# Kernel tuning notes

Measured on AMD Instinct MI355X. Metric: run time of the kernel, lower is better.

The kernel has to match this reference:

```python
import jax, jax.numpy as jnp
import numpy as np

B, N, IN_DIM, MEM, HID = 8, 512, 768, 300, 64
LEAKY_SLOPE = 0.01
NEG_INF = -1e30


def setup_inputs() -> dict:
    key = jax.random.key(0)
    ks = jax.random.split(key, 8)
    adj = jax.random.randint(ks[0], (B, N, N), 0, 2).astype(jnp.float32)
    feature = jax.random.normal(ks[1], (B, N, IN_DIM), dtype=jnp.float32)
    # GCN projection W[0]: Linear(in_dim, mem_dim)
    W_w = jax.random.normal(ks[2], (MEM, IN_DIM), dtype=jnp.float32) / np.sqrt(IN_DIM)
    W_b = jax.random.normal(ks[3], (MEM,), dtype=jnp.float32) * 0.02
    # afcs: Linear(2*mem, hidden) -> ReLU -> Linear(hidden, 1)
    a1_w = jax.random.normal(ks[4], (HID, 2 * MEM), dtype=jnp.float32) / np.sqrt(2 * MEM)
    a1_b = jax.random.normal(ks[5], (HID,), dtype=jnp.float32) * 0.02
    a2_w = jax.random.normal(ks[6], (1, HID), dtype=jnp.float32) / np.sqrt(HID)
    a2_b = jax.random.normal(ks[7], (1,), dtype=jnp.float32) * 0.02
    return {"adj": adj, "feature": feature, "W_w": W_w, "W_b": W_b,
            "a1_w": a1_w, "a1_b": a1_b, "a2_w": a2_w, "a2_b": a2_b}


def reference(adj, feature, W_w, W_b, a1_w, a1_b, a2_w, a2_b):
    # num_layers = 1 -> single GAT layer, no inter-layer dropout (eval math)
    b, n, _ = adj.shape
    h = feature @ W_w.T + W_b                      # [B,N,MEM]
    # a_input[:, i*N+j] = concat(h_i, h_j); decompose Linear(2*mem, hid)
    s_i = h @ a1_w[:, :MEM].T                      # [B,N,HID] (contribution of h_i)
    s_j = h @ a1_w[:, MEM:].T                      # [B,N,HID] (contribution of h_j)
    pre = s_i[:, :, None, :] + s_j[:, None, :, :] + a1_b   # [B,N,N,HID]
    e = jax.nn.relu(pre) @ a2_w[0] + a2_b[0]       # [B,N,N] (second afcs linear)
    e = jnp.where(e >= 0, e, LEAKY_SLOPE * e)      # LeakyReLU(0.01)
    # mask_logits + softmax over the FLATTENED N*N dim (dim=1 of [B, N*N])
    dmask = adj.reshape(b, -1)
    logits = e.reshape(b, -1) * dmask + (1.0 - dmask) * NEG_INF
    attention = jax.nn.softmax(logits, axis=1).reshape(b, n, n)
    out = jnp.einsum('bij,bjd->bid', attention, h)  # attention.bmm(h)
    return out
```

## Files before the change

### kernel.cpp

```cpp
#include <hip/hip_runtime.h>

#define NEGINF (-1e30f)

typedef __attribute__((ext_vector_type(8))) short short8;
typedef __attribute__((ext_vector_type(4))) float f32x4;

__device__ inline float waveRedSum(float v){
  #pragma unroll
  for (int o = 32; o > 0; o >>= 1) v += __shfl_down(v, o, 64);
  return v;
}
__device__ inline float waveRedMax(float v){
  #pragma unroll
  for (int o = 32; o > 0; o >>= 1) v = fmaxf(v, __shfl_down(v, o, 64));
  return v;
}
__device__ inline float4 f4z(){ return make_float4(0.f,0.f,0.f,0.f); }
#define F4C(v, c) ((c)==0?(v).x:(c)==1?(v).y:(c)==2?(v).z:(v).w)

__device__ inline unsigned short f2bf(float f){
  unsigned u = __float_as_uint(f);
  unsigned r = u + 0x7fffu + ((u >> 16) & 1u);
  return (unsigned short)(r >> 16);
}
__device__ inline float bf2f(unsigned short h){
  return __uint_as_float(((unsigned)h) << 16);
}

__global__ __launch_bounds__(256) void k1_h(const float* __restrict__ A,
                                            const float* __restrict__ W,
                                            const float* __restrict__ Wb,
                                            float* __restrict__ H){
  __shared__ short Ah[2][64*40];
  __shared__ short Al[2][64*40];
  __shared__ short Bh[2][64*40];
  __shared__ short Bl[2][64*40];
  const int fid = blockIdx.x;
  const int wl  = (fid & 7) * 40 + (fid >> 3);
  const int y = wl / 5, x = wl % 5;
  const int m0 = y * 64, c0 = x * 64;
  const int t = threadIdx.x;
  const int lane = t & 63, w = t >> 6;
  const int wr = w >> 1, wc = w & 1;
  const int srow = t >> 2, kq = (t & 3) * 8;
  const bool bok = (c0 + srow) < 300;
  const float* Arow = A + (size_t)(m0 + srow) * 768 + kq;
  const float* Wrow = W + (size_t)(c0 + srow) * 768 + kq;
  float4 ra0, ra1, rb0, rb1;
#define K1_LD(kt) { \
    ra0 = *(const float4*)(Arow + (kt)); \
    ra1 = *(const float4*)(Arow + (kt) + 4); \
    rb0 = bok ? *(const float4*)(Wrow + (kt)) : f4z(); \
    rb1 = bok ? *(const float4*)(Wrow + (kt) + 4) : f4z(); }
  K1_LD(0)
  f32x4 acc[2][2];
  #pragma unroll
  for (int i = 0; i < 2; i++)
    #pragma unroll
    for (int j = 0; j < 2; j++)
      acc[i][j] = (f32x4){0.f, 0.f, 0.f, 0.f};
  const int fr = lane & 15;
  const int fk = (lane >> 4) * 8;
  int p = 0;
  for (int tile = 0; tile < 24; ++tile){
    {
      float av[8] = {ra0.x, ra0.y, ra0.z, ra0.w, ra1.x, ra1.y, ra1.z, ra1.w};
      float bv[8] = {rb0.x, rb0.y, rb0.z, rb0.w, rb1.x, rb1.y, rb1.z, rb1.w};
      short8 vah, val_, vbh, vbl;
      #pragma unroll
      for (int i = 0; i < 8; i++){
        unsigned short hh = f2bf(av[i]);
        vah[i] = (short)hh;
        val_[i] = (short)f2bf(av[i] - bf2f(hh));
        unsigned short gh = f2bf(bv[i]);
        vbh[i] = (short)gh;
        vbl[i] = (short)f2bf(bv[i] - bf2f(gh));
      }
      const int o = srow * 40 + kq;
      *(short8*)&Ah[p][o] = vah;
      *(short8*)&Al[p][o] = val_;
      *(short8*)&Bh[p][o] = vbh;
      *(short8*)&Bl[p][o] = vbl;
    }
    __syncthreads();
    if (tile < 23) K1_LD((tile + 1) * 32)
    {
      const int a0o = (wr*32      + fr) * 40 + fk;
      const int a1o = (wr*32 + 16 + fr) * 40 + fk;
      const int b0o = (wc*32      + fr) * 40 + fk;
      const int b1o = (wc*32 + 16 + fr) * 40 + fk;
      short8 fAh[2], fAl[2], fBh[2], fBl[2];
      fAh[0] = *(short8*)&Ah[p][a0o]; fAh[1] = *(short8*)&Ah[p][a1o];
      fAl[0] = *(short8*)&Al[p][a0o]; fAl[1] = *(short8*)&Al[p][a1o];
      fBh[0] = *(short8*)&Bh[p][b0o]; fBh[1] = *(short8*)&Bh[p][b1o];
      fBl[0] = *(short8*)&Bl[p][b0o]; fBl[1] = *(short8*)&Bl[p][b1o];
      #pragma unroll
      for (int sm = 0; sm < 2; sm++)
        #pragma unroll
        for (int sn = 0; sn < 2; sn++){
          acc[sm][sn] = __builtin_amdgcn_mfma_f32_16x16x32_bf16(fAh[sm], fBh[sn], acc[sm][sn], 0, 0, 0);
          acc[sm][sn] = __builtin_amdgcn_mfma_f32_16x16x32_bf16(fAh[sm], fBl[sn], acc[sm][sn], 0, 0, 0);
          acc[sm][sn] = __builtin_amdgcn_mfma_f32_16x16x32_bf16(fAl[sm], fBh[sn], acc[sm][sn], 0, 0, 0);
        }
    }
    p ^= 1;
  }
#undef K1_LD
  const int crow = (lane >> 4) * 4;
  const int ccol = lane & 15;
  #pragma unroll
  for (int sn = 0; sn < 2; sn++){
    const int gcol = c0 + wc*32 + sn*16 + ccol;
    if (gcol < 300){
      const float bi = Wb[gcol];
      #pragma unroll
      for (int sm = 0; sm < 2; sm++){
        const int rbase = m0 + wr*32 + sm*16 + crow;
        #pragma unroll
        for (int r = 0; r < 4; r++)
          H[(size_t)(rbase + r) * 300 + gcol] = acc[sm][sn][r] + bi;
      }
    }
  }
}

__global__ __launch_bounds__(256) void k2_s(const float* __restrict__ Hm,
                                            const float* __restrict__ a1w,
                                            const float* __restrict__ a1b,
                                            float* __restrict__ S){
  __shared__ float As[2][32*40];
  __shared__ float Bs[2][32*136];
  const int bid = blockIdx.x;
  const int y = (bid & 7) * 16 + (bid >> 3);
  const int m0 = y * 32;
  const int t = threadIdx.x;
  const int tr4 = (t >> 5) * 4, tc = t & 31;
  const int arow = t >> 3, akq = t & 7;
  const int bn = t & 127, bkh = t >> 7;
  const float* brp = (bn < 64) ? &a1w[(size_t)bn * 600] : &a1w[(size_t)(bn - 64) * 600 + 300];
  float4 ha, b4[4];
  float4 acc[4];
  #pragma unroll
  for (int i = 0; i < 4; i++) acc[i] = f4z();
#define K2_LD(kt) { \
    const int ka = (kt) + akq*4; \
    ha = (ka < 300) ? *(const float4*)&Hm[(size_t)(m0 + arow)*300 + ka] : f4z(); \
    _Pragma("unroll") \
    for (int j = 0; j < 4; j++){ \
      const int kb = (kt) + bkh*16 + 4*j; \
      b4[j] = (kb < 300) ? *(const float4*)&brp[kb] : f4z(); \
    } }
  K2_LD(0)
  int p = 0;
  for (int tile = 0; tile < 10; ++tile){
    #pragma unroll
    for (int jj = 0; jj < 4; jj++)
      As[p][(akq*4 + jj)*40 + ((((arow>>2) ^ akq) & 7) << 2) + (arow & 3)] = F4C(ha, jj);
    #pragma unroll
    for (int jj = 0; jj < 16; jj++){
      const int kl = bkh*16 + jj;
      const int swb = (kl >> 2) & 7;
      Bs[p][kl*136 + (((bn>>2) ^ swb) << 2) + (bn & 3)] = F4C(b4[jj>>2], jj&3);
    }
    __syncthreads();
    if (tile < 9) K2_LD((tile + 1) * 32)
    #pragma unroll
    for (int kk = 0; kk < 32; kk++){
      const int sw = (kk >> 2) & 7;
      const float4 av = *(const float4*)&As[p][kk*40 + (((t>>5) ^ sw) << 2)];
      const float4 bv = *(const float4*)&Bs[p][kk*136 + ((tc ^ sw) << 2)];
      acc[0].x += av.x*bv.x; acc[0].y += av.x*bv.y; acc[0].z += av.x*bv.z; acc[0].w += av.x*bv.w;
      acc[1].x += av.y*bv.x; acc[1].y += av.y*bv.y; acc[1].z += av.y*bv.z; acc[1].w += av.y*bv.w;
      acc[2].x += av.z*bv.x; acc[2].y += av.z*bv.y; acc[2].z += av.z*bv.z; acc[2].w += av.z*bv.w;
      acc[3].x += av.w*bv.x; acc[3].y += av.w*bv.y; acc[3].z += av.w*bv.z; acc[3].w += av.w*bv.w;
    }
    p ^= 1;
  }
#undef K2_LD
  const int tc4 = tc * 4;
  float4 bi = f4z();
  if (tc4 < 64) bi = *(const float4*)&a1b[tc4];
  #pragma unroll
  for (int i = 0; i < 4; i++){
    float4 o = make_float4(acc[i].x+bi.x, acc[i].y+bi.y, acc[i].z+bi.z, acc[i].w+bi.w);
    *(float4*)&S[(size_t)(m0 + tr4 + i) * 128 + tc4] = o;
  }
}

__global__ __launch_bounds__(256) void k3_logits(const float* __restrict__ S,
                                                 const float* __restrict__ adj,
                                                 const float* __restrict__ a2w,
                                                 const float* __restrict__ a2b,
                                                 float* __restrict__ L,
                                                 float* __restrict__ bm,
                                                 float* __restrict__ bs){
  __shared__ float sj_s[64*68];
  __shared__ float w_s[64];
  __shared__ float redm[4];
  __shared__ float reds[4];
  __shared__ float smax;
  const int b  = blockIdx.z;
  const int i0 = blockIdx.y * 32;
  const int j0 = blockIdx.x * 64;
  const int t  = threadIdx.x;
  const int j = t & 63, iq = t >> 6;
  if (t < 16) *(float4*)&w_s[t*4] = *(const float4*)&a2w[t*4];
  #pragma unroll
  for (int q = 0; q < 4; q++){
    int c = t + q*256; int r = c >> 4, c4 = c & 15;
    *(float4*)&sj_s[r*68 + c4*4] = *(const float4*)&S[(size_t)(b*512 + j0 + r)*128 + 64 + c4*4];
  }
  float vsi[8];
  #pragma unroll
  for (int r = 0; r < 8; r++)
    vsi[r] = S[(size_t)(b*512 + i0 + r*4 + iq) * 128 + j];
  __syncthreads();
  const float a2bv = a2b[0];
  float accA[8][4];
  #pragma unroll
  for (int r = 0; r < 8; r++)
    #pragma unroll
    for (int c = 0; c < 4; c++) accA[r][c] = 0.f;
  #pragma unroll
  for (int k4 = 0; k4 < 16; k4++){
    const float4 sj4 = *(const float4*)&sj_s[j*68 + k4*4];
    const float4 w4  = *(const float4*)&w_s[k4*4];
    #pragma unroll
    for (int c = 0; c < 4; c++){
      const int k = k4*4 + c;
      const float sjc = F4C(sj4, c);
      const float wc  = F4C(w4, c);
      #pragma unroll
      for (int r = 0; r < 8; r++){
        const float s = __int_as_float(__builtin_amdgcn_readlane(__float_as_int(vsi[r]), k));
        accA[r][c] += fmaxf(s + sjc, 0.f) * wc;
      }
    }
  }
  float l_arr[8];
  float locmax = -3e38f;
  #pragma unroll
  for (int r = 0; r < 8; r++){
    const int i = r*4 + iq;
    float e = ((accA[r][0] + accA[r][1]) + (accA[r][2] + accA[r][3])) + a2bv;
    e = (e >= 0.f) ? e : 0.01f * e;
    size_t idxg = (size_t)(b*512 + i0 + i)*512 + j0 + j;
    float l = (adj[idxg] != 0.f) ? e : NEGINF;
    l_arr[r] = l;
    L[idxg] = l;
    locmax = fmaxf(locmax, l);
  }
  float m = waveRedMax(locmax);
  if ((t & 63) == 0) redm[t >> 6] = m;
  __syncthreads();
  if (t == 0) smax = fmaxf(fmaxf(redm[0], redm[1]), fmaxf(redm[2], redm[3]));
  __syncthreads();
  const float mb = smax;
  float sacc = 0.f;
  #pragma unroll
  for (int r = 0; r < 8; r++) sacc += __expf(l_arr[r] - mb);
  sacc = waveRedSum(sacc);
  if ((t & 63) == 0) reds[t >> 6] = sacc;
  __syncthreads();
  if (t == 0){
    const int bid = (blockIdx.z * 16 + blockIdx.y) * 8 + blockIdx.x;
    bm[bid] = mb;
    bs[bid] = (reds[0] + reds[1]) + (reds[2] + reds[3]);
  }
}

__global__ __launch_bounds__(128) void k6_red(const float* __restrict__ bm,
                                              const float* __restrict__ bs,
                                              float* __restrict__ sums,
                                              float* __restrict__ maxg){
  const int b = blockIdx.x, t = threadIdx.x;
  const float m = bm[b*128 + t];
  float mm = waveRedMax(m);
  __shared__ float r2m[2];
  __shared__ float mgs;
  if ((t & 63) == 0) r2m[t >> 6] = mm;
  __syncthreads();
  if (t == 0) mgs = fmaxf(r2m[0], r2m[1]);
  __syncthreads();
  const float mg = mgs;
  float v = bs[b*128 + t] * __expf(m - mg);
  v = waveRedSum(v);
  __shared__ float r2s[2];
  if ((t & 63) == 0) r2s[t >> 6] = v;
  __syncthreads();
  if (t == 0){ sums[b] = r2s[0] + r2s[1]; maxg[b] = mg; }
}

__global__ __launch_bounds__(256) void k7_out(const float* __restrict__ Lr,
                                              const float* __restrict__ Hm,
                                              const float* __restrict__ sums,
                                              const float* __restrict__ maxg,
                                              float* __restrict__ out){
  __shared__ short Ah[2][64*40];
  __shared__ short Al[2][64*40];
  __shared__ short Bh[2][64*40];
  __shared__ short Bl[2][64*40];
  const int fid = blockIdx.x;
  const int b = fid & 7, idx = fid >> 3;
  const int y = idx / 5, x = idx % 5;
  const int m0 = y * 64, c0 = x * 64;
  const int t = threadIdx.x;
  const int lane = t & 63, wv = t >> 6;
  const int wr = wv >> 1, wc = wv & 1;
  const float mx = maxg[b];
  const int srow = t >> 2, kq = (t & 3) * 8;
  const float* Lrow = Lr + (size_t)(b*512 + m0 + srow) * 512 + kq;
  const int tk = t >> 4, tn = t & 15;
  const int k0 = tk * 2, n0 = tn * 4;
  const int gcolB = c0 + n0;
  const bool bok = gcolB < 300;
  float4 ra0, ra1, hb0, hb1;
#define K7_LD(kt) { \
    ra0 = *(const float4*)(Lrow + (kt)); \
    ra1 = *(const float4*)(Lrow + (kt) + 4); \
    const float* hr = Hm + (size_t)(b*512 + (kt) + k0) * 300 + gcolB; \
    hb0 = bok ? *(const float4*)hr : f4z(); \
    hb1 = bok ? *(const float4*)(hr + 300) : f4z(); }
  K7_LD(0)
  f32x4 acc[2][2];
  #pragma unroll
  for (int i = 0; i < 2; i++)
    #pragma unroll
    for (int jj = 0; jj < 2; jj++)
      acc[i][jj] = (f32x4){0.f, 0.f, 0.f, 0.f};
  const int fr = lane & 15;
  const int fg = lane >> 4;
  const int fk = fg * 8;
  int p = 0;
  for (int tile = 0; tile < 16; ++tile){
    {
      float av[8] = {ra0.x, ra0.y, ra0.z, ra0.w, ra1.x, ra1.y, ra1.z, ra1.w};
      short8 vah, val_;
      #pragma unroll
      for (int i = 0; i < 8; i++){
        const float e = __expf(av[i] - mx);
        unsigned short hh = f2bf(e);
        vah[i] = (short)hh;
        val_[i] = (short)f2bf(e - bf2f(hh));
      }
      const int o = srow * 40 + kq;
      *(short8*)&Ah[p][o] = vah;
      *(short8*)&Al[p][o] = val_;
      #pragma unroll
      for (int i = 0; i < 4; i++){
        const float v0 = F4C(hb0, i), v1 = F4C(hb1, i);
        const unsigned short h0 = f2bf(v0), h1 = f2bf(v1);
        const unsigned short l0 = f2bf(v0 - bf2f(h0)), l1 = f2bf(v1 - bf2f(h1));
        const int n = n0 + i;
        const int kbs = (k0 >> 3) ^ (n & 3);
        const int soff = n*40 + kbs*8 + (k0 & 7);
        *(unsigned*)&Bh[p][soff] = (unsigned)h0 | ((unsigned)h1 << 16);
        *(unsigned*)&Bl[p][soff] = (unsigned)l0 | ((unsigned)l1 << 16);
      }
    }
    __syncthreads();
    if (tile < 15) K7_LD((tile + 1) * 32)
    {
      const int a0o = (wr*32      + fr) * 40 + fk;
      const int a1o = (wr*32 + 16 + fr) * 40 + fk;
      const int nb0 = wc*32      + fr;
      const int nb1 = wc*32 + 16 + fr;
      const int b0o = nb0*40 + (fg ^ (nb0 & 3)) * 8;
      const int b1o = nb1*40 + (fg ^ (nb1 & 3)) * 8;
      short8 fAh[2], fAl[2], fBh[2], fBl[2];
      fAh[0] = *(short8*)&Ah[p][a0o]; fAh[1] = *(short8*)&Ah[p][a1o];
      fAl[0] = *(short8*)&Al[p][a0o]; fAl[1] = *(short8*)&Al[p][a1o];
      fBh[0] = *(short8*)&Bh[p][b0o]; fBh[1] = *(short8*)&Bh[p][b1o];
      fBl[0] = *(short8*)&Bl[p][b0o]; fBl[1] = *(short8*)&Bl[p][b1o];
      #pragma unroll
      for (int sm = 0; sm < 2; sm++)
        #pragma unroll
        for (int sn = 0; sn < 2; sn++){
          acc[sm][sn] = __builtin_amdgcn_mfma_f32_16x16x32_bf16(fAh[sm], fBh[sn], acc[sm][sn], 0, 0, 0);
          acc[sm][sn] = __builtin_amdgcn_mfma_f32_16x16x32_bf16(fAh[sm], fBl[sn], acc[sm][sn], 0, 0, 0);
          acc[sm][sn] = __builtin_amdgcn_mfma_f32_16x16x32_bf16(fAl[sm], fBh[sn], acc[sm][sn], 0, 0, 0);
        }
    }
    p ^= 1;
  }
#undef K7_LD
  const float invs = 1.0f / sums[b];
  const int crow = (lane >> 4) * 4;
  const int ccol = lane & 15;
  #pragma unroll
  for (int sn = 0; sn < 2; sn++){
    const int gcol = c0 + wc*32 + sn*16 + ccol;
    if (gcol < 300){
      #pragma unroll
      for (int sm = 0; sm < 2; sm++){
        const int rbase = m0 + wr*32 + sm*16 + crow;
        #pragma unroll
        for (int r = 0; r < 4; r++)
          out[(size_t)(b*512 + rbase + r) * 300 + gcol] = acc[sm][sn][r] * invs;
      }
    }
  }
}

extern "C" void kernel_launch(void* const* d_in, const int* in_sizes, int n_in,
                              void* d_out, int out_size, void* d_ws, size_t ws_size,
                              hipStream_t stream){
  const float* adj  = (const float*)d_in[0];
  const float* feat = (const float*)d_in[1];
  const float* Ww   = (const float*)d_in[2];
  const float* Wb   = (const float*)d_in[3];
  const float* a1w  = (const float*)d_in[4];
  const float* a1b  = (const float*)d_in[5];
  const float* a2w  = (const float*)d_in[6];
  const float* a2b  = (const float*)d_in[7];
  float* out = (float*)d_out;
  char* ws = (char*)d_ws;

  float* H    = (float*)(ws + 0);
  float* S    = (float*)(ws + 4915200);
  float* L    = (float*)(ws + 7012352);
  float* bm   = (float*)(ws + 15400960);
  float* bs   = (float*)(ws + 15405056);
  float* sums = (float*)(ws + 15409152);
  float* maxg = (float*)(ws + 15409216);

  k1_h     <<<dim3(320),      dim3(256), 0, stream>>>(feat, Ww, Wb, H);
  k2_s     <<<dim3(128),      dim3(256), 0, stream>>>(H, a1w, a1b, S);
  k3_logits<<<dim3(8, 16, 8), dim3(256), 0, stream>>>(S, adj, a2w, a2b, L, bm, bs);
  k6_red   <<<dim3(8),        dim3(128), 0, stream>>>(bm, bs, sums, maxg);
  k7_out   <<<dim3(320),      dim3(256), 0, stream>>>(L, H, sums, maxg, out);
}
```

Before: 83.23 us.

## Use split-bf16 MFMA for the attention-score projection GEMM

The second GEMM kernel (H times the two halves of a1_w) moves from a scalar FP32 outer-product loop to MFMA 16x16x32 bf16 instructions. Each FP32 operand is split into high and low bf16 parts and three products are summed to keep near-FP32 accuracy. Tiles become 64x64 with 4 waves, and the grid is remapped so the two column halves go to separate blocks. The cost is the conversion work and extra LDS traffic, in exchange for much higher matrix throughput. This kernel is likely a small share of the total runtime.

```diff
diff --git a/kernel.cpp b/kernel.cpp
--- a/kernel.cpp
+++ b/kernel.cpp
@@ -128,62 +128,96 @@
                                             const float* __restrict__ a1w,
                                             const float* __restrict__ a1b,
                                             float* __restrict__ S){
-  __shared__ float As[2][32*40];
-  __shared__ float Bs[2][32*136];
-  const int bid = blockIdx.x;
-  const int y = (bid & 7) * 16 + (bid >> 3);
-  const int m0 = y * 32;
+  __shared__ short Ah[2][64*40];
+  __shared__ short Al[2][64*40];
+  __shared__ short Bh[2][64*40];
+  __shared__ short Bl[2][64*40];
+  const int fid = blockIdx.x;
+  const int wl  = (fid & 7) * 16 + (fid >> 3);
+  const int y = wl >> 1, x = wl & 1;
+  const int m0 = y * 64, c0 = x * 64;
   const int t = threadIdx.x;
-  const int tr4 = (t >> 5) * 4, tc = t & 31;
-  const int arow = t >> 3, akq = t & 7;
-  const int bn = t & 127, bkh = t >> 7;
-  const float* brp = (bn < 64) ? &a1w[(size_t)bn * 600] : &a1w[(size_t)(bn - 64) * 600 + 300];
-  float4 ha, b4[4];
-  float4 acc[4];
-  #pragma unroll
-  for (int i = 0; i < 4; i++) acc[i] = f4z();
+  const int lane = t & 63, w = t >> 6;
+  const int wr = w >> 1, wc = w & 1;
+  const int srow = t >> 2, kq = (t & 3) * 8;
+  const int brow = c0 + srow;
+  const float* Arow = Hm + (size_t)(m0 + srow) * 300;
+  const float* Brow = (brow < 64) ? (a1w + (size_t)brow * 600)
+                                  : (a1w + (size_t)(brow - 64) * 600 + 300);
+  float4 ra0, ra1, rb0, rb1;
 #define K2_LD(kt) { \
-    const int ka = (kt) + akq*4; \
-    ha = (ka < 300) ? *(const float4*)&Hm[(size_t)(m0 + arow)*300 + ka] : f4z(); \
-    _Pragma("unroll") \
-    for (int j = 0; j < 4; j++){ \
-      const int kb = (kt) + bkh*16 + 4*j; \
-      b4[j] = (kb < 300) ? *(const float4*)&brp[kb] : f4z(); \
-    } }
+    const int k = (kt) + kq; \
+    ra0 = (k <= 296) ? *(const float4*)(Arow + k)     : f4z(); \
+    ra1 = (k <= 292) ? *(const float4*)(Arow + k + 4) : f4z(); \
+    rb0 = (k <= 296) ? *(const float4*)(Brow + k)     : f4z(); \
+    rb1 = (k <= 292) ? *(const float4*)(Brow + k + 4) : f4z(); }
   K2_LD(0)
+  f32x4 acc[2][2];
+  #pragma unroll
+  for (int i = 0; i < 2; i++)
+    #pragma unroll
+    for (int j = 0; j < 2; j++)
+      acc[i][j] = (f32x4){0.f, 0.f, 0.f, 0.f};
+  const int fr = lane & 15;
+  const int fk = (lane >> 4) * 8;
   int p = 0;
   for (int tile = 0; tile < 10; ++tile){
-    #pragma unroll
-    for (int jj = 0; jj < 4; jj++)
-      As[p][(akq*4 + jj)*40 + ((((arow>>2) ^ akq) & 7) << 2) + (arow & 3)] = F4C(ha, jj);
-    #pragma unroll
-    for (int jj = 0; jj < 16; jj++){
-      const int kl = bkh*16 + jj;
-      const int swb = (kl >> 2) & 7;
-      Bs[p][kl*136 + (((bn>>2) ^ swb) << 2) + (bn & 3)] = F4C(b4[jj>>2], jj&3);
+    {
+      float av[8] = {ra0.x, ra0.y, ra0.z, ra0.w, ra1.x, ra1.y, ra1.z, ra1.w};
+      float bv[8] = {rb0.x, rb0.y, rb0.z, rb0.w, rb1.x, rb1.y, rb1.z, rb1.w};
+      short8 vah, val_, vbh, vbl;
+      #pragma unroll
+      for (int i = 0; i < 8; i++){
+        unsigned short hh = f2bf(av[i]);
+        vah[i] = (short)hh;
+        val_[i] = (short)f2bf(av[i] - bf2f(hh));
+        unsigned short gh = f2bf(bv[i]);
+        vbh[i] = (short)gh;
+        vbl[i] = (short)f2bf(bv[i] - bf2f(gh));
+      }
+      const int o = srow * 40 + kq;
+      *(short8*)&Ah[p][o] = vah;
+      *(short8*)&Al[p][o] = val_;
+      *(short8*)&Bh[p][o] = vbh;
+      *(short8*)&Bl[p][o] = vbl;
     }
     __syncthreads();
     if (tile < 9) K2_LD((tile + 1) * 32)
-    #pragma unroll
-    for (int kk = 0; kk < 32; kk++){
-      const int sw = (kk >> 2) & 7;
-      const float4 av = *(const float4*)&As[p][kk*40 + (((t>>5) ^ sw) << 2)];
-      const float4 bv = *(const float4*)&Bs[p][kk*136 + ((tc ^ sw) << 2)];
-      acc[0].x += av.x*bv.x; acc[0].y += av.x*bv.y; acc[0].z += av.x*bv.z; acc[0].w += av.x*bv.w;
-      acc[1].x += av.y*bv.x; acc[1].y += av.y*bv.y; acc[1].z += av.y*bv.z; acc[1].w += av.y*bv.w;
-      acc[2].x += av.z*bv.x; acc[2].y += av.z*bv.y; acc[2].z += av.z*bv.z; acc[2].w += av.z*bv.w;
-      acc[3].x += av.w*bv.x; acc[3].y += av.w*bv.y; acc[3].z += av.w*bv.z; acc[3].w += av.w*bv.w;
+    {
+      const int a0o = (wr*32      + fr) * 40 + fk;
+      const int a1o = (wr*32 + 16 + fr) * 40 + fk;
+      const int b0o = (wc*32      + fr) * 40 + fk;
+      const int b1o = (wc*32 + 16 + fr) * 40 + fk;
+      short8 fAh[2], fAl[2], fBh[2], fBl[2];
+      fAh[0] = *(short8*)&Ah[p][a0o]; fAh[1] = *(short8*)&Ah[p][a1o];
+      fAl[0] = *(short8*)&Al[p][a0o]; fAl[1] = *(short8*)&Al[p][a1o];
+      fBh[0] = *(short8*)&Bh[p][b0o]; fBh[1] = *(short8*)&Bh[p][b1o];
+      fBl[0] = *(short8*)&Bl[p][b0o]; fBl[1] = *(short8*)&Bl[p][b1o];
+      #pragma unroll
+      for (int sm = 0; sm < 2; sm++)
+        #pragma unroll
+        for (int sn = 0; sn < 2; sn++){
+          acc[sm][sn] = __builtin_amdgcn_mfma_f32_16x16x32_bf16(fAh[sm], fBh[sn], acc[sm][sn], 0, 0, 0);
+          acc[sm][sn] = __builtin_amdgcn_mfma_f32_16x16x32_bf16(fAh[sm], fBl[sn], acc[sm][sn], 0, 0, 0);
+          acc[sm][sn] = __builtin_amdgcn_mfma_f32_16x16x32_bf16(fAl[sm], fBh[sn], acc[sm][sn], 0, 0, 0);
+        }
     }
     p ^= 1;
   }
 #undef K2_LD
-  const int tc4 = tc * 4;
-  float4 bi = f4z();
-  if (tc4 < 64) bi = *(const float4*)&a1b[tc4];
-  #pragma unroll
-  for (int i = 0; i < 4; i++){
-    float4 o = make_float4(acc[i].x+bi.x, acc[i].y+bi.y, acc[i].z+bi.z, acc[i].w+bi.w);
-    *(float4*)&S[(size_t)(m0 + tr4 + i) * 128 + tc4] = o;
+  const int crow = (lane >> 4) * 4;
+  const int ccol = lane & 15;
+  #pragma unroll
+  for (int sn = 0; sn < 2; sn++){
+    const int gcol = c0 + wc*32 + sn*16 + ccol;
+    const float bi = (gcol < 64) ? a1b[gcol] : 0.f;
+    #pragma unroll
+    for (int sm = 0; sm < 2; sm++){
+      const int rbase = m0 + wr*32 + sm*16 + crow;
+      #pragma unroll
+      for (int r = 0; r < 4; r++)
+        S[(size_t)(rbase + r) * 128 + gcol] = acc[sm][sn][r] + bi;
+    }
   }
 }
 
```

After: 77.26 us, median of 2. 7.2% less time.
